# Optimization experiments

Hardware: AMD Instinct MI355X
Metric: run time of the kernel (lower is better)

## Reference

```python
import jax, jax.numpy as jnp
import numpy as np

B, T, NE, H = 4, 1024, 1024, 16
HS = NE // H  # 64
EPS = 0.00064


def setup_inputs() -> dict:
    key = jax.random.key(0)
    ks = jax.random.split(key, 30)
    def rn(k, shape, s):
        return jax.random.normal(k, shape, jnp.float32) * s
    d = {}
    d["x"] = jax.random.normal(ks[0], (B, T, NE), jnp.float32)
    d["time_maa_x"] = jax.random.uniform(ks[1], (NE,), jnp.float32)
    d["time_maa"] = jax.random.uniform(ks[2], (4, 1, 1, NE), jnp.float32)
    d["maa_w1"] = rn(ks[3], (128, NE), 0.02)   # 4 * D_MIX_LORA=32
    d["maa_w2"] = rn(ks[4], (4, 32, NE), 0.02)
    d["decay_w1"] = rn(ks[5], (64, NE), 0.02)
    d["decay_w2"] = rn(ks[6], (64, NE), 0.02)
    d["aaa_w1"] = rn(ks[7], (16, NE), 0.02)
    d["aaa_w2"] = rn(ks[8], (16, NE), 0.02)
    d["kkk_w1"] = rn(ks[9], (16, NE), 0.02)
    d["kkk_w2"] = rn(ks[10], (16, NE), 0.02)
    d["gate_w1"] = rn(ks[11], (128, NE), 0.02)
    d["gate_w2"] = rn(ks[12], (128, NE), 0.02)
    d["ma_w1"] = rn(ks[13], (16, NE), 0.02)
    d["ma_w2"] = rn(ks[14], (16, NE), 0.02)
    d["mk_w1"] = rn(ks[15], (16, NE), 0.02)
    d["mk_w2"] = rn(ks[16], (16, NE), 0.02)
    d["time_decay"] = jnp.linspace(-6.5, -1.5, NE, dtype=jnp.float32)  # decay_speed + 0.5 shape
    d["time_faaaa"] = rn(ks[17], (NE,), 0.02)
    d["time_aaaaa"] = rn(ks[18], (NE,), 0.02)
    d["time_misc_a"] = rn(ks[19], (NE,), 0.02)
    d["time_misc_k"] = rn(ks[20], (NE,), 0.02)
    d["Wr"] = rn(ks[21], (NE, NE), 0.5 / NE ** 0.5)
    d["Wk"] = rn(ks[22], (NE, NE), 0.05 / NE ** 0.5)
    d["Wv"] = rn(ks[23], (NE, NE), 0.5 / NE ** 0.5)
    d["Wo"] = rn(ks[24], (NE, NE), 1.0 / NE ** 0.5)
    d["ln_w"] = jnp.ones((NE,), jnp.float32)
    d["ln_b"] = jnp.zeros((NE,), jnp.float32)
    return d


def _forward(x, time_maa_x, time_maa, maa_w1, maa_w2, decay_w1, decay_w2,
             aaa_w1, aaa_w2, kkk_w1, kkk_w2, gate_w1, gate_w2,
             ma_w1, ma_w2, mk_w1, mk_w2, time_decay, time_faaaa, time_aaaaa,
             time_misc_a, time_misc_k, Wr, Wk, Wv, Wo, ln_w, ln_b):
    Bx, Tx, C = x.shape
    # token-shift delta: xx[t] = x[t-1] - x[t], with x[-1] = 0
    xx = jnp.pad(x, ((0, 0), (1, 0), (0, 0)))[:, :Tx] - x
    mix = x + xx * time_maa_x
    lo = jnp.tanh(jnp.einsum('btc,dc->btd', mix, maa_w1)).reshape(Bx, Tx, 4, 32)
    lo = jnp.einsum('btgk,gkc->gbtc', lo, maa_w2)           # [4,B,T,C]
    xm = x[None] + xx[None] * (lo + time_maa)               # time_maa broadcasts [4,1,1,C]
    xrg, xwa, xk, xv = xm[0], xm[1], xm[2], xm[3]

    r = xrg @ Wr.T
    g = jnp.tanh(xrg @ gate_w1.T) @ gate_w2
    k = xk @ Wk.T
    v = xv @ Wv.T
    w2 = jnp.tanh(xwa @ decay_w1.T) @ decay_w2
    w = -jax.nn.softplus(-(time_decay + w2)) - 0.5
    kk = k + jnp.tanh(xk @ kkk_w1.T) @ kkk_w2
    kkh = kk.reshape(Bx, Tx, H, HS)
    kk = (kkh / jnp.maximum(jnp.linalg.norm(kkh, axis=-1, keepdims=True), 1e-12)).reshape(Bx, Tx, C)
    a = jax.nn.sigmoid(time_aaaaa + (xwa @ aaa_w1.T) @ aaa_w2)
    ma = jax.nn.sigmoid(time_misc_a + (xwa @ ma_w1.T) @ ma_w2)
    k = k * ma + k * a * (1.0 - ma)
    mk = jax.nn.sigmoid(time_misc_k + (xk @ mk_w1.T) @ mk_w2)
    k = k * jnp.exp(w * mk)
    b = -kk * a

    # RWKV7 delta-rule recurrence: per-(B,H) HSxHS matrix state, scan over T
    def to_th(t):
        return t.reshape(Bx, Tx, H, HS).transpose(1, 0, 2, 3)  # [T,B,H,HS]
    qt, wt, kt, vt, at, bt = map(to_th, (r, w, k, v, kk, b))
    wt = jnp.exp(-jnp.exp(wt))

    def step(s, inp):
        q_, w_, k_, v_, a_, b_ = inp
        sa = jnp.einsum('bhij,bhj->bhi', s, a_)
        s = s * w_[:, :, None, :] + sa[..., None] * b_[:, :, None, :] + v_[..., None] * k_[:, :, None, :]
        return s, jnp.einsum('bhij,bhj->bhi', s, q_)

    s0 = jnp.zeros((Bx, H, HS, HS), x.dtype)
    _, y = jax.lax.scan(step, s0, (qt, wt, kt, vt, at, bt))
    y = y.transpose(1, 0, 2, 3).reshape(Bx, Tx, C)

    # GroupNorm with H groups, eps=0.00064
    yg = y.reshape(Bx, Tx, H, HS)
    mu = yg.mean(-1, keepdims=True)
    var = ((yg - mu) ** 2).mean(-1, keepdims=True)
    y = ((yg - mu) / jnp.sqrt(var + EPS)).reshape(Bx, Tx, C) * ln_w + ln_b

    # per-head bonus: (r.k * faaaa) v
    rk = (r.reshape(Bx, Tx, H, HS) * k.reshape(Bx, Tx, H, HS) * time_faaaa.reshape(H, HS)).sum(-1, keepdims=True)
    y = y + (rk * v.reshape(Bx, Tx, H, HS)).reshape(Bx, Tx, C)
    return (y * g) @ Wo.T


def reference(x, time_maa_x, time_maa, maa_w1, maa_w2, decay_w1, decay_w2,
              aaa_w1, aaa_w2, kkk_w1, kkk_w2, gate_w1, gate_w2,
              ma_w1, ma_w2, mk_w1, mk_w2, time_decay, time_faaaa, time_aaaaa,
              time_misc_a, time_misc_k, Wr, Wk, Wv, Wo, ln_w, ln_b):
    return _forward(x, time_maa_x, time_maa, maa_w1, maa_w2, decay_w1, decay_w2,
                    aaa_w1, aaa_w2, kkk_w1, kkk_w2, gate_w1, gate_w2,
                    ma_w1, ma_w2, mk_w1, mk_w2, time_decay, time_faaaa, time_aaaaa,
                    time_misc_a, time_misc_k, Wr, Wk, Wv, Wo, ln_w, ln_b)
```

## Files before the change

### kernel.cpp

```cpp
#include <hip/hip_runtime.h>
#include <cstdint>
#include <cstddef>

#define BB   4
#define TT   1024
#define CC   1024
#define HH   16
#define HSS  64
#define NNtok 4096
#define EPSGN 0.00064f
#define W2TS 192

typedef unsigned short bf16u;
typedef __attribute__((ext_vector_type(8))) short short8;
typedef __attribute__((ext_vector_type(4))) float f32x4;
#define SLOT 4194304ull

__device__ __forceinline__ float bf2f(bf16u u){
  union { unsigned int i; float f; } cv; cv.i = ((unsigned int)u) << 16; return cv.f;
}
__device__ __forceinline__ unsigned short f2bfbits(unsigned int x){
  return (unsigned short)((x + 0x7fffu + ((x >> 16) & 1u)) >> 16);
}
__device__ __forceinline__ bf16u f2bf(float f){
  union { float f; unsigned int i; } cv; cv.f = f;
  return f2bfbits(cv.i);
}
__device__ __forceinline__ void ld4bf(const bf16u* p, float* o){
  ushort4 u = *reinterpret_cast<const ushort4*>(p);
  o[0]=bf2f(u.x); o[1]=bf2f(u.y); o[2]=bf2f(u.z); o[3]=bf2f(u.w);
}
__device__ __forceinline__ void st4bf(bf16u* p, const float* v){
  ushort4 u; u.x=f2bf(v[0]); u.y=f2bf(v[1]); u.z=f2bf(v[2]); u.w=f2bf(v[3]);
  *reinterpret_cast<ushort4*>(p) = u;
}
__device__ __forceinline__ unsigned short f2h(float f){
  union { _Float16 h; unsigned short s; } c; c.h = (_Float16)f; return c.s;
}
__device__ __forceinline__ void st4h(bf16u* p, const float* v){
  ushort4 u; u.x=f2h(v[0]); u.y=f2h(v[1]); u.z=f2h(v[2]); u.w=f2h(v[3]);
  *reinterpret_cast<ushort4*>(p) = u;
}
__device__ __forceinline__ void ld4f(const float* p, float* o){
  float4 v = *reinterpret_cast<const float4*>(p);
  o[0]=v.x; o[1]=v.y; o[2]=v.z; o[3]=v.w;
}
__device__ __forceinline__ float sigm(float x){ return 1.f / (1.f + expf(-x)); }

__device__ __forceinline__ float bflo(unsigned int u){
  union { unsigned int i; float f; } c; c.i = u << 16; return c.f;
}
__device__ __forceinline__ float bfhi(unsigned int u){
  union { unsigned int i; float f; } c; c.i = u & 0xffff0000u; return c.f;
}
__device__ __forceinline__ float hlo(unsigned int u){
  union { unsigned short s; _Float16 h; } c; c.s = (unsigned short)(u & 0xffffu); return (float)c.h;
}
__device__ __forceinline__ float hhi(unsigned int u){
  union { unsigned short s; _Float16 h; } c; c.s = (unsigned short)(u >> 16); return (float)c.h;
}
__device__ __forceinline__ float hval(unsigned short s){
  union { unsigned short s; _Float16 h; } c; c.s = s; return (float)c.h;
}
__device__ __forceinline__ float dot4(const float* x, const float* y){
  return (x[0]*y[0] + x[1]*y[1]) + (x[2]*y[2] + x[3]*y[3]);
}

template<int CTRL>
__device__ __forceinline__ float dpp_add(float v){
  union { float f; int i; } a, b;
  a.f = v;
  b.i = __builtin_amdgcn_update_dpp(0, a.i, CTRL, 0xF, 0xF, true);
  return v + b.f;
}
__device__ __forceinline__ float red16(float v){
  v = dpp_add<0xB1>(v);
  v = dpp_add<0x4E>(v);
  v = dpp_add<0x124>(v);
  v = dpp_add<0x128>(v);
  return v;
}
__device__ __forceinline__ float red32(float v){
  v = red16(v);
  union { float f; int i; } x, y;
  x.f = v; y.f = v;
  asm volatile("" : "+v"(y.i));
  asm volatile("v_permlane16_swap_b32 %0, %1" : "+v"(x.i), "+v"(y.i));
  return x.f + y.f;
}

__global__ __launch_bounds__(256) void k_prep(const float* __restrict__ x,
                                              const float* __restrict__ tmx,
                                              bf16u* __restrict__ MIX){
  int e = (blockIdx.x * 256 + threadIdx.x) * 4;
  int n = e >> 10;
  int c = e & (CC - 1);
  int t = n & (TT - 1);
  float xf[4]; ld4f(x + e, xf);
  float pf[4] = {0.f, 0.f, 0.f, 0.f};
  if (t > 0) ld4f(x + e - CC, pf);
  float tm[4]; ld4f(tmx + c, tm);
  float mv[4];
  #pragma unroll
  for (int i = 0; i < 4; ++i) mv[i] = xf[i] + (pf[i] - xf[i]) * tm[i];
  st4bf(MIX + e, mv);
}

__global__ __launch_bounds__(256) void k_prep_wconv(
    const float* __restrict__ x, const float* __restrict__ tmx,
    bf16u* __restrict__ MIX,
    const float* __restrict__ Wr, const float* __restrict__ Wk,
    const float* __restrict__ Wv,
    const float* __restrict__ maa_w1, const float* __restrict__ gate_w1,
    const float* __restrict__ decay_w1, const float* __restrict__ aaa_w1,
    const float* __restrict__ ma_w1, const float* __restrict__ kkk_w1,
    const float* __restrict__ mk_w1,
    const float* __restrict__ maa_w2, const float* __restrict__ decay_w2,
    bf16u* __restrict__ WrB, bf16u* __restrict__ WkB, bf16u* __restrict__ WvB,
    bf16u* __restrict__ W1B, bf16u* __restrict__ W2TB){
  int tid = threadIdx.x;
  if (blockIdx.x < 4096){
    int e = (blockIdx.x * 256 + tid) * 4;
    int n = e >> 10;
    int c = e & (CC - 1);
    int t = n & (TT - 1);
    float xf[4]; ld4f(x + e, xf);
    float pf[4] = {0.f, 0.f, 0.f, 0.f};
    if (t > 0) ld4f(x + e - CC, pf);
    float tm[4]; ld4f(tmx + c, tm);
    float mv[4];
    #pragma unroll
    for (int i = 0; i < 4; ++i) mv[i] = xf[i] + (pf[i] - xf[i]) * tm[i];
    st4bf(MIX + e, mv);
    return;
  }
  int blk = blockIdx.x - 4096;
  if (blk < 3072){
    const float* src = (blk < 1024) ? Wr : (blk < 2048) ? Wk : Wv;
    bf16u* dst = (blk < 1024) ? WrB : (blk < 2048) ? WkB : WvB;
    size_t e = (size_t)(blk & 1023) * 1024 + (size_t)tid * 4;
    float v[4]; ld4f(src + e, v);
    st4bf(dst + e, v);
  } else if (blk < 3456){
    int row = blk - 3072;
    const float* src;
    if      (row < 128) src = maa_w1   + (size_t)row * 1024;
    else if (row < 256) src = gate_w1  + (size_t)(row - 128) * 1024;
    else if (row < 320) src = decay_w1 + (size_t)(row - 256) * 1024;
    else if (row < 336) src = aaa_w1   + (size_t)(row - 320) * 1024;
    else if (row < 352) src = ma_w1    + (size_t)(row - 336) * 1024;
    else if (row < 368) src = kkk_w1   + (size_t)(row - 352) * 1024;
    else                src = mk_w1    + (size_t)(row - 368) * 1024;
    float v[4]; ld4f(src + tid * 4, v);
    st4bf(W1B + (size_t)row * 1024 + tid * 4, v);
  } else {
    int j = blk - 3456;
    const float* src = (j < 128) ? (maa_w2 + (size_t)j * 1024)
                                 : (decay_w2 + (size_t)(j - 128) * 1024);
    for (int c = tid; c < 1024; c += 256)
      W2TB[(size_t)c * W2TS + j] = f2bf(src[c]);
  }
}

#define B64_AROW 72
#define B64_ASZ (64*72)
#define B64_BSZ (128*72)
template<bool OB>
__device__ __forceinline__ void gemm_b64_body(const bf16u* __restrict__ X,
                                              const bf16u* __restrict__ WB,
                                              void* __restrict__ OUTv,
                                              int Nd, int Kd, int act_n,
                                              short* __restrict__ As,
                                              short* __restrict__ Bs,
                                              int bn0, int bm0){
  const int tid  = threadIdx.x;
  const int lane = tid & 63;
  const int wv   = tid >> 6;
  const int wm   = wv >> 1, wn = wv & 1;
  const int l15  = lane & 15;
  const int quad = lane >> 4;

  f32x4 acc[2][4];
  #pragma unroll
  for (int mi = 0; mi < 2; ++mi)
    #pragma unroll
    for (int ni = 0; ni < 4; ++ni)
      #pragma unroll
      for (int rg = 0; rg < 4; ++rg) acc[mi][ni][rg] = 0.f;

  const int ra = tid >> 2, k0a = (tid & 3) * 16;
  const int rb = tid >> 1, k0b = (tid & 1) * 32;
  const bf16u* xsrc = X + (size_t)(bm0 + ra) * Kd;
  const bf16u* wsrc = (bn0 + rb < Nd) ? WB + (size_t)(bn0 + rb) * Kd : nullptr;

  uint4 xa0 = *(const uint4*)(xsrc + k0a);
  uint4 xa1 = *(const uint4*)(xsrc + k0a + 8);
  uint4 wa0 = make_uint4(0,0,0,0), wa1 = wa0, wa2 = wa0, wa3 = wa0;
  if (wsrc){
    wa0 = *(const uint4*)(wsrc + k0b);
    wa1 = *(const uint4*)(wsrc + k0b + 8);
    wa2 = *(const uint4*)(wsrc + k0b + 16);
    wa3 = *(const uint4*)(wsrc + k0b + 24);
  }
  *(uint4*)&As[ra * B64_AROW + k0a]      = xa0;
  *(uint4*)&As[ra * B64_AROW + k0a + 8]  = xa1;
  *(uint4*)&Bs[rb * B64_AROW + k0b]      = wa0;
  *(uint4*)&Bs[rb * B64_AROW + k0b + 8]  = wa1;
  *(uint4*)&Bs[rb * B64_AROW + k0b + 16] = wa2;
  *(uint4*)&Bs[rb * B64_AROW + k0b + 24] = wa3;
  __syncthreads();

  const int NS = Kd >> 6;
  for (int s = 0; s < NS; ++s){
    const int cur = s & 1;
    if (s + 1 < NS){
      int kb = (s + 1) << 6;
      xa0 = *(const uint4*)(xsrc + kb + k0a);
      xa1 = *(const uint4*)(xsrc + kb + k0a + 8);
      if (wsrc){
        wa0 = *(const uint4*)(wsrc + kb + k0b);
        wa1 = *(const uint4*)(wsrc + kb + k0b + 8);
        wa2 = *(const uint4*)(wsrc + kb + k0b + 16);
        wa3 = *(const uint4*)(wsrc + kb + k0b + 24);
      }
    }
    #pragma unroll
    for (int kk = 0; kk < 64; kk += 32){
      short8 af[2], bfg[4];
      #pragma unroll
      for (int mi = 0; mi < 2; ++mi)
        af[mi] = *(const short8*)&As[cur*B64_ASZ + (wm*32 + mi*16 + l15) * B64_AROW + kk + quad*8];
      #pragma unroll
      for (int ni = 0; ni < 4; ++ni)
        bfg[ni] = *(const short8*)&Bs[cur*B64_BSZ + (wn*64 + ni*16 + l15) * B64_AROW + kk + quad*8];
      #pragma unroll
      for (int mi = 0; mi < 2; ++mi)
        #pragma unroll
        for (int ni = 0; ni < 4; ++ni)
          acc[mi][ni] = __builtin_amdgcn_mfma_f32_16x16x32_bf16(af[mi], bfg[ni], acc[mi][ni], 0, 0, 0);
    }
    if (s + 1 < NS){
      const int nxt = cur ^ 1;
      *(uint4*)&As[nxt*B64_ASZ + ra * B64_AROW + k0a]      = xa0;
      *(uint4*)&As[nxt*B64_ASZ + ra * B64_AROW + k0a + 8]  = xa1;
      *(uint4*)&Bs[nxt*B64_BSZ + rb * B64_AROW + k0b]      = wa0;
      *(uint4*)&Bs[nxt*B64_BSZ + rb * B64_AROW + k0b + 8]  = wa1;
      *(uint4*)&Bs[nxt*B64_BSZ + rb * B64_AROW + k0b + 16] = wa2;
      *(uint4*)&Bs[nxt*B64_BSZ + rb * B64_AROW + k0b + 24] = wa3;
      __syncthreads();
    }
  }

  #pragma unroll
  for (int mi = 0; mi < 2; ++mi){
    #pragma unroll
    for (int ni = 0; ni < 4; ++ni){
      int col = bn0 + wn*64 + ni*16 + l15;
      if (col >= Nd) continue;
      #pragma unroll
      for (int rg = 0; rg < 4; ++rg){
        int row = bm0 + wm*32 + mi*16 + quad*4 + rg;
        float v = acc[mi][ni][rg];
        if (col < act_n) v = tanhf(v);
        if (OB) ((bf16u*)OUTv)[(size_t)row * Nd + col] = f2bf(v);
        else    ((float*)OUTv)[(size_t)row * Nd + col] = v;
      }
    }
  }
}

template<bool OB>
__global__ __launch_bounds__(256) void k_gemm_b64(const bf16u* __restrict__ X,
                                                  const bf16u* __restrict__ WB,
                                                  void* __restrict__ OUTv,
                                                  int Nd, int Kd, int act_n){
  __shared__ short As[2*B64_ASZ];
  __shared__ short Bs[2*B64_BSZ];
  gemm_b64_body<OB>(X, WB, OUTv, Nd, Kd, act_n, As, Bs,
                    blockIdx.x * 128, blockIdx.y * 64);
}

#define B128_SZ (128*40)
template<bool OB>
__device__ __forceinline__ void gemm_b128_body(const bf16u* __restrict__ X,
                                               const bf16u* __restrict__ WB,
                                               void* __restrict__ OUTv,
                                               int Nd, int Kd, int act_n,
                                               short* __restrict__ As,
                                               short* __restrict__ Bs,
                                               int bn0, int bm0){
  const int tid  = threadIdx.x;
  const int lane = tid & 63;
  const int wv   = tid >> 6;
  const int wm   = wv >> 1, wn = wv & 1;
  const int l15  = lane & 15;
  const int quad = lane >> 4;

  f32x4 acc[4][4];
  #pragma unroll
  for (int mi = 0; mi < 4; ++mi)
    #pragma unroll
    for (int ni = 0; ni < 4; ++ni)
      #pragma unroll
      for (int rg = 0; rg < 4; ++rg) acc[mi][ni][rg] = 0.f;

  const int r    = tid >> 1;
  const int half = (tid & 1) * 16;
  const bf16u* wsrc = (bn0 + r < Nd) ? WB + (size_t)(bn0 + r) * Kd : nullptr;
  const bf16u* xsrc = X + (size_t)(bm0 + r) * Kd;

  uint4 xa = *(const uint4*)(xsrc + half);
  uint4 xb = *(const uint4*)(xsrc + half + 8);
  uint4 wa = make_uint4(0,0,0,0), wb = wa;
  if (wsrc){
    wa = *(const uint4*)(wsrc + half);
    wb = *(const uint4*)(wsrc + half + 8);
  }
  *(uint4*)&As[r * 40 + half]     = xa;
  *(uint4*)&As[r * 40 + half + 8] = xb;
  *(uint4*)&Bs[r * 40 + half]     = wa;
  *(uint4*)&Bs[r * 40 + half + 8] = wb;
  __syncthreads();

  const int NK = Kd >> 5;
  for (int k = 0; k < NK; ++k){
    const int cur = k & 1;
    if (k + 1 < NK){
      int k0 = (k + 1) << 5;
      xa = *(const uint4*)(xsrc + k0 + half);
      xb = *(const uint4*)(xsrc + k0 + half + 8);
      if (wsrc){
        wa = *(const uint4*)(wsrc + k0 + half);
        wb = *(const uint4*)(wsrc + k0 + half + 8);
      }
    }
    short8 af[4], bfg[4];
    #pragma unroll
    for (int mi = 0; mi < 4; ++mi)
      af[mi] = *(const short8*)&As[cur*B128_SZ + (wm*64 + mi*16 + l15) * 40 + quad*8];
    #pragma unroll
    for (int ni = 0; ni < 4; ++ni)
      bfg[ni] = *(const short8*)&Bs[cur*B128_SZ + (wn*64 + ni*16 + l15) * 40 + quad*8];
    #pragma unroll
    for (int mi = 0; mi < 4; ++mi)
      #pragma unroll
      for (int ni = 0; ni < 4; ++ni)
        acc[mi][ni] = __builtin_amdgcn_mfma_f32_16x16x32_bf16(af[mi], bfg[ni], acc[mi][ni], 0, 0, 0);
    if (k + 1 < NK){
      const int nxt = cur ^ 1;
      *(uint4*)&As[nxt*B128_SZ + r * 40 + half]     = xa;
      *(uint4*)&As[nxt*B128_SZ + r * 40 + half + 8] = xb;
      *(uint4*)&Bs[nxt*B128_SZ + r * 40 + half]     = wa;
      *(uint4*)&Bs[nxt*B128_SZ + r * 40 + half + 8] = wb;
      __syncthreads();
    }
  }

  #pragma unroll
  for (int mi = 0; mi < 4; ++mi){
    #pragma unroll
    for (int ni = 0; ni < 4; ++ni){
      int col = bn0 + wn*64 + ni*16 + l15;
      if (col >= Nd) continue;
      #pragma unroll
      for (int rg = 0; rg < 4; ++rg){
        int row = bm0 + wm*64 + mi*16 + quad*4 + rg;
        float v = acc[mi][ni][rg];
        if (col < act_n) v = tanhf(v);
        if (OB) ((bf16u*)OUTv)[(size_t)row * Nd + col] = f2bf(v);
        else    ((float*)OUTv)[(size_t)row * Nd + col] = v;
      }
    }
  }
}

__global__ __launch_bounds__(256) void k_gemm_b128_rkv(const bf16u* __restrict__ X0,
                                                       const bf16u* __restrict__ X2,
                                                       const bf16u* __restrict__ X3,
                                                       const bf16u* __restrict__ WrB,
                                                       const bf16u* __restrict__ WkB,
                                                       const bf16u* __restrict__ WvB,
                                                       bf16u* __restrict__ R,
                                                       bf16u* __restrict__ K0,
                                                       bf16u* __restrict__ V){
  __shared__ short As[2*B128_SZ];
  __shared__ short Bs[2*B128_SZ];
  const int z = blockIdx.z;
  const int bn0 = blockIdx.x * 128, bm0 = blockIdx.y * 128;
  if (z == 0)      gemm_b128_body<true>(X0, WrB, R,  CC, CC, 0, As, Bs, bn0, bm0);
  else if (z == 1) gemm_b128_body<true>(X2, WkB, K0, CC, CC, 0, As, Bs, bn0, bm0);
  else             gemm_b128_body<true>(X3, WvB, V,  CC, CC, 0, As, Bs, bn0, bm0);
}

__global__ __launch_bounds__(256) void k_gemm_b64_lora(const bf16u* __restrict__ X0,
                                                       const bf16u* __restrict__ X1,
                                                       const bf16u* __restrict__ X2,
                                                       const bf16u* __restrict__ W1B,
                                                       bf16u* __restrict__ GT,
                                                       bf16u* __restrict__ P1,
                                                       bf16u* __restrict__ P2){
  __shared__ short As[2*B64_ASZ];
  __shared__ short Bs[2*B64_BSZ];
  const int z = blockIdx.z;
  const int bm0 = blockIdx.y * 64;
  if (z == 0)
    gemm_b64_body<true>(X0, W1B + 128*1024, GT, 128, CC, 128, As, Bs, 0, bm0);
  else if (z == 1)
    gemm_b64_body<true>(X1, W1B + 256*1024, P1, 96, CC, 64, As, Bs, 0, bm0);
  else
    gemm_b64_body<true>(X2, W1B + 352*1024, P2, 32, CC, 16, As, Bs, 0, bm0);
}

template<int KD, int EP>
__device__ __forceinline__ void gemm_nn_body(const bf16u* __restrict__ A, int lda,
                                             const bf16u* __restrict__ BT, int koff,
                                             bf16u* __restrict__ OUT,
                                             const float* __restrict__ x,
                                             const float* __restrict__ tma_g,
                                             short* __restrict__ As,
                                             short* __restrict__ Bs,
                                             int bn0, int bm0){
  const int tid  = threadIdx.x;
  const int lane = tid & 63;
  const int wv   = tid >> 6;
  const int wm   = wv >> 1, wn = wv & 1;
  const int l15  = lane & 15;
  const int quad = lane >> 4;

  for (int idx = tid; idx < 128 * (KD / 8); idx += 256){
    int r  = idx / (KD / 8);
    int kc = (idx % (KD / 8)) * 8;
    *(uint4*)&As[r * (KD + 8) + kc] =
        *(const uint4*)(A + (size_t)(bm0 + r) * lda + kc);
  }
  for (int idx = tid; idx < 128 * (KD / 8); idx += 256){
    int cc_ = idx / (KD / 8);
    int kc  = (idx % (KD / 8)) * 8;
    *(uint4*)&Bs[cc_ * (KD + 8) + kc] =
        *(const uint4*)(BT + (size_t)(bn0 + cc_) * W2TS + koff + kc);
  }
  __syncthreads();

  f32x4 acc[4][4];
  #pragma unroll
  for (int mi = 0; mi < 4; ++mi)
    #pragma unroll
    for (int ni = 0; ni < 4; ++ni)
      #pragma unroll
      for (int rg = 0; rg < 4; ++rg) acc[mi][ni][rg] = 0.f;

  #pragma unroll
  for (int kk = 0; kk < KD; kk += 32){
    short8 af[4], bfg[4];
    #pragma unroll
    for (int mi = 0; mi < 4; ++mi)
      af[mi] = *(const short8*)&As[(wm*64 + mi*16 + l15) * (KD + 8) + kk + quad*8];
    #pragma unroll
    for (int ni = 0; ni < 4; ++ni)
      bfg[ni] = *(const short8*)&Bs[(wn*64 + ni*16 + l15) * (KD + 8) + kk + quad*8];
    #pragma unroll
    for (int mi = 0; mi < 4; ++mi)
      #pragma unroll
      for (int ni = 0; ni < 4; ++ni)
        acc[mi][ni] = __builtin_amdgcn_mfma_f32_16x16x32_bf16(af[mi], bfg[ni], acc[mi][ni], 0, 0, 0);
  }

  #pragma unroll
  for (int mi = 0; mi < 4; ++mi){
    #pragma unroll
    for (int ni = 0; ni < 4; ++ni){
      int col = bn0 + wn*64 + ni*16 + l15;
      float tm = (EP == 1) ? tma_g[col] : 0.f;
      #pragma unroll
      for (int rg = 0; rg < 4; ++rg){
        int row = bm0 + wm*64 + mi*16 + quad*4 + rg;
        float v = acc[mi][ni][rg];
        if (EP == 1){
          float xv = x[(size_t)row * CC + col];
          float xp = ((row & (TT - 1)) == 0) ? 0.f : x[(size_t)row * CC + col - CC];
          v = xv + (xp - xv) * (v + tm);
        }
        OUT[(size_t)row * CC + col] = f2bf(v);
      }
    }
  }
}

template<int KD, int EP>
__global__ __launch_bounds__(256) void k_gemm_nn_b(const bf16u* __restrict__ A, int lda,
                                                   const bf16u* __restrict__ BT, int koff,
                                                   bf16u* __restrict__ OUT,
                                                   const float* __restrict__ x,
                                                   const float* __restrict__ tma_g){
  __shared__ short As[128 * (KD + 8)];
  __shared__ short Bs[128 * (KD + 8)];
  gemm_nn_body<KD, EP>(A, lda, BT, koff, OUT, x, tma_g, As, Bs,
                       blockIdx.x * 128, blockIdx.y * 128);
}

__global__ __launch_bounds__(256) void k_gemm_nn_b4(const bf16u* __restrict__ LO,
                                                    const bf16u* __restrict__ BT,
                                                    bf16u* __restrict__ X0base,
                                                    const float* __restrict__ x,
                                                    const float* __restrict__ tmaa){
  __shared__ short As[128 * 40];
  __shared__ short Bs[128 * 40];
  const int z = blockIdx.z;
  gemm_nn_body<32, 1>(LO + z*32, 128, BT, z*32, X0base + (size_t)z*SLOT,
                      x, tmaa + (size_t)z*CC, As, Bs,
                      blockIdx.x * 128, blockIdx.y * 128);
}

template<bool OB>
__global__ __launch_bounds__(256) void k_gemm_mfma(const bf16u* __restrict__ X,
                                                   const float* __restrict__ Wa,
                                                   const float* __restrict__ Wb,
                                                   const float* __restrict__ Wc,
                                                   int na, int nab,
                                                   void* __restrict__ OUTv,
                                                   int Nd, int Kd, int act_n){
  __shared__ short As[128 * 40];
  __shared__ short Bs[128 * 40];
  const int tid  = threadIdx.x;
  const int lane = tid & 63;
  const int wv   = tid >> 6;
  const int wm   = wv >> 1, wn = wv & 1;
  const int bn0  = blockIdx.x * 128;
  const int bm0  = blockIdx.y * 128;
  const int l15  = lane & 15;
  const int quad = lane >> 4;

  f32x4 acc[4][4];
  #pragma unroll
  for (int mi = 0; mi < 4; ++mi)
    #pragma unroll
    for (int ni = 0; ni < 4; ++ni)
      #pragma unroll
      for (int rg = 0; rg < 4; ++rg) acc[mi][ni][rg] = 0.f;

  const int r    = tid >> 1;
  const int half = (tid & 1) * 16;

  int rr = bn0 + r;
  const float* wsrc = nullptr;
  if (rr < na)        wsrc = Wa + (size_t)rr * Kd;
  else if (rr < nab)  wsrc = Wb + (size_t)(rr - na) * Kd;
  else if (rr < Nd)   wsrc = Wc + (size_t)(rr - nab) * Kd;
  const bf16u* xsrc = X + (size_t)(bm0 + r) * Kd;

  for (int k0 = 0; k0 < Kd; k0 += 32){
    uint4 xa = *(const uint4*)(xsrc + k0 + half);
    uint4 xb = *(const uint4*)(xsrc + k0 + half + 8);
    uint4 w0 = make_uint4(0,0,0,0), w1 = w0, w2 = w0, w3 = w0;
    if (wsrc){
      w0 = *(const uint4*)(wsrc + k0 + half);
      w1 = *(const uint4*)(wsrc + k0 + half + 4);
      w2 = *(const uint4*)(wsrc + k0 + half + 8);
      w3 = *(const uint4*)(wsrc + k0 + half + 12);
    }
    union { unsigned short s[8]; uint4 v; } p0, p1;
    p0.s[0]=f2bfbits(w0.x); p0.s[1]=f2bfbits(w0.y); p0.s[2]=f2bfbits(w0.z); p0.s[3]=f2bfbits(w0.w);
    p0.s[4]=f2bfbits(w1.x); p0.s[5]=f2bfbits(w1.y); p0.s[6]=f2bfbits(w1.z); p0.s[7]=f2bfbits(w1.w);
    p1.s[0]=f2bfbits(w2.x); p1.s[1]=f2bfbits(w2.y); p1.s[2]=f2bfbits(w2.z); p1.s[3]=f2bfbits(w2.w);
    p1.s[4]=f2bfbits(w3.x); p1.s[5]=f2bfbits(w3.y); p1.s[6]=f2bfbits(w3.z); p1.s[7]=f2bfbits(w3.w);

    *(uint4*)&As[r * 40 + half]     = xa;
    *(uint4*)&As[r * 40 + half + 8] = xb;
    *(uint4*)&Bs[r * 40 + half]     = p0.v;
    *(uint4*)&Bs[r * 40 + half + 8] = p1.v;
    __syncthreads();

    short8 af[4], bfg[4];
    #pragma unroll
    for (int mi = 0; mi < 4; ++mi)
      af[mi] = *(const short8*)&As[(wm*64 + mi*16 + l15) * 40 + quad*8];
    #pragma unroll
    for (int ni = 0; ni < 4; ++ni)
      bfg[ni] = *(const short8*)&Bs[(wn*64 + ni*16 + l15) * 40 + quad*8];
    #pragma unroll
    for (int mi = 0; mi < 4; ++mi)
      #pragma unroll
      for (int ni = 0; ni < 4; ++ni)
        acc[mi][ni] = __builtin_amdgcn_mfma_f32_16x16x32_bf16(af[mi], bfg[ni], acc[mi][ni], 0, 0, 0);
    __syncthreads();
  }

  #pragma unroll
  for (int mi = 0; mi < 4; ++mi){
    #pragma unroll
    for (int ni = 0; ni < 4; ++ni){
      int col = bn0 + wn*64 + ni*16 + l15;
      if (col >= Nd) continue;
      #pragma unroll
      for (int rg = 0; rg < 4; ++rg){
        int row = bm0 + wm*64 + mi*16 + quad*4 + rg;
        float v = acc[mi][ni][rg];
        if (col < act_n) v = tanhf(v);
        if (OB) ((bf16u*)OUTv)[(size_t)row * Nd + col] = f2bf(v);
        else    ((float*)OUTv)[(size_t)row * Nd + col] = v;
      }
    }
  }
}

template<int KD, int EP>
__global__ __launch_bounds__(256) void k_gemm_nn(const bf16u* __restrict__ A, int lda,
                                                 const float* __restrict__ B,
                                                 bf16u* __restrict__ OUT,
                                                 const float* __restrict__ x,
                                                 const float* __restrict__ tma_g){
  __shared__ short As[128 * (KD + 8)];
  __shared__ short Bs[128 * (KD + 8)];
  const int tid  = threadIdx.x;
  const int lane = tid & 63;
  const int wv   = tid >> 6;
  const int wm   = wv >> 1, wn = wv & 1;
  const int bn0  = blockIdx.x * 128;
  const int bm0  = blockIdx.y * 128;
  const int l15  = lane & 15;
  const int quad = lane >> 4;

  for (int idx = tid; idx < 128 * (KD / 8); idx += 256){
    int r  = idx / (KD / 8);
    int kc = (idx % (KD / 8)) * 8;
    *(uint4*)&As[r * (KD + 8) + kc] =
        *(const uint4*)(A + (size_t)(bm0 + r) * lda + kc);
  }
  for (int idx = tid; idx < KD * 128; idx += 256){
    int k = idx >> 7, c = idx & 127;
    Bs[c * (KD + 8) + k] = (short)f2bf(B[(size_t)k * CC + bn0 + c]);
  }
  __syncthreads();

  f32x4 acc[4][4];
  #pragma unroll
  for (int mi = 0; mi < 4; ++mi)
    #pragma unroll
    for (int ni = 0; ni < 4; ++ni)
      #pragma unroll
      for (int rg = 0; rg < 4; ++rg) acc[mi][ni][rg] = 0.f;

  #pragma unroll
  for (int kk = 0; kk < KD; kk += 32){
    short8 af[4], bfg[4];
    #pragma unroll
    for (int mi = 0; mi < 4; ++mi)
      af[mi] = *(const short8*)&As[(wm*64 + mi*16 + l15) * (KD + 8) + kk + quad*8];
    #pragma unroll
    for (int ni = 0; ni < 4; ++ni)
      bfg[ni] = *(const short8*)&Bs[(wn*64 + ni*16 + l15) * (KD + 8) + kk + quad*8];
    #pragma unroll
    for (int mi = 0; mi < 4; ++mi)
      #pragma unroll
      for (int ni = 0; ni < 4; ++ni)
        acc[mi][ni] = __builtin_amdgcn_mfma_f32_16x16x32_bf16(af[mi], bfg[ni], acc[mi][ni], 0, 0, 0);
  }

  #pragma unroll
  for (int mi = 0; mi < 4; ++mi){
    #pragma unroll
    for (int ni = 0; ni < 4; ++ni){
      int col = bn0 + wn*64 + ni*16 + l15;
      float tm = (EP == 1) ? tma_g[col] : 0.f;
      #pragma unroll
      for (int rg = 0; rg < 4; ++rg){
        int row = bm0 + wm*64 + mi*16 + quad*4 + rg;
        float v = acc[mi][ni][rg];
        if (EP == 1){
          float xv = x[(size_t)row * CC + col];
          float xp = ((row & (TT - 1)) == 0) ? 0.f : x[(size_t)row * CC + col - CC];
          v = xv + (xp - xv) * (v + tm);
        }
        OUT[(size_t)row * CC + col] = f2bf(v);
      }
    }
  }
}

template<int WMODE>
__global__ __launch_bounds__(256) void k_elem(bf16u* __restrict__ K0,
    const bf16u* __restrict__ P1, const bf16u* __restrict__ P2,
    const bf16u* __restrict__ W2A,
    const float* __restrict__ kw2, const float* __restrict__ aw2,
    const float* __restrict__ maw2, const float* __restrict__ mkw2,
    const float* __restrict__ td,  const float* __restrict__ taa,
    const float* __restrict__ tma, const float* __restrict__ tmk,
    const float* __restrict__ faaaa,
    bf16u* __restrict__ KKN, bf16u* __restrict__ Bb, bf16u* __restrict__ UX,
    float* __restrict__ WF,
    bf16u* __restrict__ Rq, float* __restrict__ Dsc, float* __restrict__ RKsc,
    const float* __restrict__ Wo, const float* __restrict__ gate_w2,
    bf16u* __restrict__ WoB, bf16u* __restrict__ GW2T){
  int tid = threadIdx.x;
  if (blockIdx.x >= 1024){
    int blk = blockIdx.x - 1024;
    if (blk < 1024){
      size_t e = ((size_t)blk * 256 + tid) * 4;
      float v[4]; ld4f(Wo + e, v);
      st4bf(WoB + e, v);
    } else {
      int c = (blk - 1024) * 2 + (tid >> 7);
      int j = tid & 127;
      GW2T[(size_t)c * 128 + j] = f2bf(gate_w2[(size_t)j * CC + c]);
    }
    return;
  }
  int n0 = blockIdx.x * 4;
  __shared__ float at_l[4][16], mat_l[4][16], kt_l[4][16], mkt_l[4][16];
  {
    int grp = tid >> 6, q = tid & 63, tt = q >> 4, j = q & 15;
    if (grp == 0)      at_l[tt][j]  = bf2f(P1[(size_t)(n0+tt)*96 + 64 + j]);
    else if (grp == 1) mat_l[tt][j] = bf2f(P1[(size_t)(n0+tt)*96 + 80 + j]);
    else if (grp == 2) kt_l[tt][j]  = bf2f(P2[(size_t)(n0+tt)*32 + j]);
    else               mkt_l[tt][j] = bf2f(P2[(size_t)(n0+tt)*32 + 16 + j]);
  }
  __syncthreads();
  int c  = tid * 4;
  int h  = tid >> 4;
  int lg = tid & 15;

  float kkk[4][4], aa[4][4], mam[4][4], mkm[4][4];
  #pragma unroll
  for (int tt = 0; tt < 4; ++tt)
    #pragma unroll
    for (int i = 0; i < 4; ++i){ kkk[tt][i]=0; aa[tt][i]=0; mam[tt][i]=0; mkm[tt][i]=0; }

  #pragma unroll 4
  for (int j = 0; j < 16; ++j){
    float wk[4], wa[4], wm[4], wq[4];
    ld4f(kw2  + (size_t)j*CC + c, wk);
    ld4f(aw2  + (size_t)j*CC + c, wa);
    ld4f(maw2 + (size_t)j*CC + c, wm);
    ld4f(mkw2 + (size_t)j*CC + c, wq);
    #pragma unroll
    for (int tt = 0; tt < 4; ++tt){
      float s1 = kt_l[tt][j], s2 = at_l[tt][j], s3 = mat_l[tt][j], s4 = mkt_l[tt][j];
      #pragma unroll
      for (int i = 0; i < 4; ++i){
        kkk[tt][i] += s1 * wk[i];
        aa[tt][i]  += s2 * wa[i];
        mam[tt][i] += s3 * wm[i];
        mkm[tt][i] += s4 * wq[i];
      }
    }
  }

  float td4[4], taa4[4], tma4[4], tmk4[4], fa4[4];
  ld4f(td + c, td4); ld4f(taa + c, taa4); ld4f(tma + c, tma4); ld4f(tmk + c, tmk4);
  ld4f(faaaa + c, fa4);

#define ELEM_TOKEN(TT_, E_, A_, B_, KF_, WD_) do{ \
    float k0a[4]; ld4bf(K0 + (E_), k0a); \
    float w2a[4]; ld4bf(W2A + (E_), w2a); \
    float ssq = 0.f; \
    _Pragma("unroll") \
    for (int i = 0; i < 4; ++i){ A_[i] = k0a[i] + kkk[TT_][i]; ssq += A_[i]*A_[i]; } \
    ssq = red16(ssq); \
    float rinv = 1.f / fmaxf(sqrtf(ssq), 1e-12f); \
    float outw_[4]; \
    _Pragma("unroll") \
    for (int i = 0; i < 4; ++i){ \
      float z  = td4[i] + w2a[i]; \
      float nz = -z; \
      float sp = (nz > 15.f) ? nz : log1pf(expf(nz)); \
      float w  = -sp - 0.5f; \
      float av  = sigm(taa4[i] + aa[TT_][i]); \
      float mav = sigm(tma4[i] + mam[TT_][i]); \
      float mkv = sigm(tmk4[i] + mkm[TT_][i]); \
      A_[i] *= rinv; \
      B_[i]  = -A_[i] * av; \
      KF_[i] = k0a[i] * (mav + av * (1.f - mav)) * expf(w * mkv); \
      float ou = -expf(w); \
      outw_[i] = ou; \
      if (WMODE == 1) WD_[i] = __expf(ou);               \
      else            WD_[i] = __expf(hval(f2h(ou)));    \
    } \
    st4bf(Bb + (E_), B_); \
    st4bf(K0 + (E_), KF_); \
    if (WMODE == 1) *(float4*)(WF + (E_)) = make_float4(WD_[0], WD_[1], WD_[2], WD_[3]); \
    else            st4h(UX + (E_), outw_); \
  }while(0)

  #pragma unroll
  for (int p = 0; p < 2; ++p){
    const int ttE = 2*p, ttO = ttE + 1;
    size_t eE = (size_t)(n0 + ttE) * CC + c;
    size_t eO = eE + CC;
    float aE[4], bE[4], kfE[4], wdE[4];
    float aO[4], bO[4], kfO[4], wdO[4];
    ELEM_TOKEN(ttE, eE, aE, bE, kfE, wdE);
    ELEM_TOKEN(ttO, eO, aO, bO, kfO, wdO);
    st4bf(KKN + eE, aE);

    float rE[4], rO[4];
    ld4bf(Rq + eE, rE); ld4bf(Rq + eO, rO);

    float rkE = red16(rE[0]*kfE[0]*fa4[0] + rE[1]*kfE[1]*fa4[1]
                    + rE[2]*kfE[2]*fa4[2] + rE[3]*kfE[3]*fa4[3]);
    float rkO = red16(rO[0]*kfO[0]*fa4[0] + rO[1]*kfO[1]*fa4[1]
                    + rO[2]*kfO[2]*fa4[2] + rO[3]*kfO[3]*fa4[3]);

    float c1 = red16(dot4(bE, aO));
    float d  = red16(dot4(kfE, aO));
    float u1[4];
    #pragma unroll
    for (int i = 0; i < 4; ++i) u1[i] = wdE[i]*aO[i] + c1*aE[i];
    st4bf(KKN + eO, u1);

    float cq = red16(dot4(bE, rE));
    float e1 = red16(dot4(kfE, rE));
    float qe[4];
    #pragma unroll
    for (int i = 0; i < 4; ++i) qe[i] = wdE[i]*rE[i] + cq*aE[i];
    st4bf(Rq + eE, qe);

    float cz  = red16(dot4(bO, rO));
    float e21 = red16(dot4(kfO, rO));
    float z[4];
    #pragma unroll
    for (int i = 0; i < 4; ++i) z[i] = wdO[i]*rO[i] + cz*aO[i];
    float cy  = red16(dot4(bE, z));
    float e20 = red16(dot4(kfE, z));
    float qo[4];
    #pragma unroll
    for (int i = 0; i < 4; ++i) qo[i] = wdE[i]*z[i] + cy*aE[i];
    st4bf(Rq + eO, qo);

    if (lg == 0){
      size_t pr = (size_t)((n0 + ttE) >> 1);
      float4 dv; dv.x = d; dv.y = e1; dv.z = e20; dv.w = e21;
      *(float4*)(Dsc + (pr * HH + h) * 4) = dv;
      RKsc[(size_t)(n0 + ttE) * HH + h] = rkE;
      RKsc[(size_t)(n0 + ttO) * HH + h] = rkO;
    }
  }
#undef ELEM_TOKEN
}

template<int WMODE>
__global__ __launch_bounds__(256) void k_rec(const bf16u* __restrict__ Qp,
                                             const bf16u* __restrict__ WT,
                                             const float* __restrict__ WF,
                                             const bf16u* __restrict__ KFt,
                                             const bf16u* __restrict__ Vt,
                                             const bf16u* __restrict__ Aa,
                                             const bf16u* __restrict__ Bv,
                                             const float* __restrict__ Dsc,
                                             bf16u* __restrict__ Y){
  const int p   = blockIdx.x;
  const int g   = (p & 7) | ((p >> 6) << 3);
  const int oct = (p >> 3) & 7;
  const int b   = g >> 4;
  const int h   = g & 15;
  const int tid = threadIdx.x;
  const int l31 = tid & 31;
  const int i   = oct * 8 + (tid >> 5);
  const size_t base0 = (size_t)(b * TT) * CC + h * HSS;
  const size_t colb  = base0 + l31 * 2;
  const size_t rowb  = base0 + i;
  const size_t dscb  = ((size_t)(b * (TT/2)) * HH + h) * 4;

  float S0 = 0.f, S1 = 0.f;

  unsigned int qEA,qOA,aEA,uOA,kEA,kOA,bEA,bOA,wEA,wOA; float2 fEA,fOA; unsigned short vEA,vOA; float4 dA;
  unsigned int qEB,qOB,aEB,uOB,kEB,kOB,bEB,bOB,wEB,wOB; float2 fEB,fOB; unsigned short vEB,vOB; float4 dB;
  unsigned int qEC,qOC,aEC,uOC,kEC,kOC,bEC,bOC,wEC,wOC; float2 fEC,fOC; unsigned short vEC,vOC; float4 dC;
  unsigned int qED,qOD,aED,uOD,kED,kOD,bED,bOD,wED,wOD; float2 fED,fOD; unsigned short vED,vOD; float4 dD;

#define PL(S, T_) do{ \
    size_t cE_ = colb + (size_t)(T_) * CC, cO_ = cE_ + CC; \
    qE##S = *(const unsigned int*)(Qp  + cE_); qO##S = *(const unsigned int*)(Qp  + cO_); \
    aE##S = *(const unsigned int*)(Aa  + cE_); uO##S = *(const unsigned int*)(Aa  + cO_); \
    kE##S = *(const unsigned int*)(KFt + cE_); kO##S = *(const unsigned int*)(KFt + cO_); \
    bE##S = *(const unsigned int*)(Bv  + cE_); bO##S = *(const unsigned int*)(Bv  + cO_); \
    if (WMODE == 1){ \
      fE##S = *(const float2*)(WF + cE_); fO##S = *(const float2*)(WF + cO_); \
    } else { \
      wE##S = *(const unsigned int*)(WT + cE_); wO##S = *(const unsigned int*)(WT + cO_); \
    } \
    vE##S = Vt[rowb + (size_t)(T_) * CC]; \
    vO##S = Vt[rowb + (size_t)(T_ + 1) * CC]; \
    d##S  = *(const float4*)(Dsc + dscb + (size_t)((T_) >> 1) * (HH*4)); \
  }while(0)

#define PSTEP(S, T_) do{ \
    float a0=bflo(aE##S), a1=bfhi(aE##S); \
    float u0=bflo(uO##S), u1=bfhi(uO##S); \
    float g0=bflo(qE##S), g1=bfhi(qE##S); \
    float o0=bflo(qO##S), o1=bfhi(qO##S); \
    float pE_ = fmaf(S1, a1, S0 * a0); \
    float pO_ = fmaf(S1, u1, S0 * u0); \
    float yE_ = fmaf(S1, g1, S0 * g0); \
    float yO_ = fmaf(S1, o1, S0 * o0); \
    pE_ = red32(pE_); \
    pO_ = red32(pO_); \
    yE_ = red32(yE_); \
    yO_ = red32(yO_); \
    float vEf = bf2f(vE##S), vOf = bf2f(vO##S); \
    float saE = pE_; \
    float saO = fmaf(d##S.x, vEf, pO_); \
    float ypE = fmaf(d##S.y, vEf, yE_); \
    float ypO = fmaf(d##S.z, vEf, fmaf(d##S.w, vOf, yO_)); \
    float k0=bflo(kE##S), k1=bfhi(kE##S); \
    float b0=bflo(bE##S), b1=bfhi(bE##S); \
    float w0, w1; \
    if (WMODE == 1){ w0=fE##S.x; w1=fE##S.y; } \
    else { w0=__expf(hlo(wE##S)); w1=__expf(hhi(wE##S)); } \
    S0 = fmaf(S0, w0, fmaf(saE, b0, vEf * k0)); \
    S1 = fmaf(S1, w1, fmaf(saE, b1, vEf * k1)); \
    float ko0=bflo(kO##S), ko1=bfhi(kO##S); \
    float bo0=bflo(bO##S), bo1=bfhi(bO##S); \
    float wo0, wo1; \
    if (WMODE == 1){ wo0=fO##S.x; wo1=fO##S.y; } \
    else { wo0=__expf(hlo(wO##S)); wo1=__expf(hhi(wO##S)); } \
    S0 = fmaf(S0, wo0, fmaf(saO, bo0, vOf * ko0)); \
    S1 = fmaf(S1, wo1, fmaf(saO, bo1, vOf * ko1)); \
    if (l31 == 0){ \
      Y[rowb + (size_t)(T_) * CC]     = f2bf(ypE); \
      Y[rowb + (size_t)(T_ + 1) * CC] = f2bf(ypO); \
    } \
  }while(0)

  PL(A, 0); PL(B, 2); PL(C, 4); PL(D, 6);
  for (int t = 0; t < TT; t += 8){
    PSTEP(A, t);
    if (t + 8  < TT) PL(A, t + 8);
    PSTEP(B, t + 2);
    if (t + 10 < TT) PL(B, t + 10);
    PSTEP(C, t + 4);
    if (t + 12 < TT) PL(C, t + 12);
    PSTEP(D, t + 6);
    if (t + 14 < TT) PL(D, t + 14);
  }
#undef PL
#undef PSTEP
}

__global__ __launch_bounds__(256) void k_post(const bf16u* __restrict__ Y,
                                              const bf16u* __restrict__ Vt,
                                              const bf16u* __restrict__ GV,
                                              const float* __restrict__ lnw,
                                              const float* __restrict__ lnb,
                                              const float* __restrict__ RKsc,
                                              bf16u* __restrict__ YG){
  int n = blockIdx.x, tid = threadIdx.x;
  int c = tid * 4;
  size_t e = (size_t)n * CC + c;

  float ya[4]; ld4bf(Y + e, ya);
  float s = ya[0] + ya[1] + ya[2] + ya[3];
  s = red16(s);
  float mu = s * (1.f / 64.f);
  float d[4], vs = 0.f;
  #pragma unroll
  for (int i = 0; i < 4; ++i){ d[i] = ya[i] - mu; vs += d[i] * d[i]; }
  vs = red16(vs);
  float rstd = rsqrtf(vs * (1.f / 64.f) + EPSGN);

  float rk = RKsc[(size_t)n * HH + (tid >> 4)];

  float va[4]; ld4bf(Vt + e, va);
  float lw4[4], lb4[4];
  ld4f(lnw + c, lw4); ld4f(lnb + c, lb4);
  float g[4]; ld4bf(GV + e, g);
  float o[4];
  #pragma unroll
  for (int i = 0; i < 4; ++i){
    float yn = d[i] * rstd * lw4[i] + lb4[i] + rk * va[i];
    o[i] = yn * g[i];
  }
  st4bf(YG + e, o);
}

extern "C" void kernel_launch(void* const* d_in, const int* in_sizes, int n_in,
                              void* d_out, int out_size, void* d_ws, size_t ws_size,
                              hipStream_t stream){
  (void)in_sizes; (void)n_in; (void)out_size;
  const float* x        = (const float*)d_in[0];
  const float* tmx      = (const float*)d_in[1];
  const float* tmaa     = (const float*)d_in[2];
  const float* maa_w1   = (const float*)d_in[3];
  const float* maa_w2   = (const float*)d_in[4];
  const float* decay_w1 = (const float*)d_in[5];
  const float* decay_w2 = (const float*)d_in[6];
  const float* aaa_w1   = (const float*)d_in[7];
  const float* aaa_w2   = (const float*)d_in[8];
  const float* kkk_w1   = (const float*)d_in[9];
  const float* kkk_w2   = (const float*)d_in[10];
  const float* gate_w1  = (const float*)d_in[11];
  const float* gate_w2  = (const float*)d_in[12];
  const float* ma_w1    = (const float*)d_in[13];
  const float* ma_w2    = (const float*)d_in[14];
  const float* mk_w1    = (const float*)d_in[15];
  const float* mk_w2    = (const float*)d_in[16];
  const float* t_decay  = (const float*)d_in[17];
  const float* t_faaaa  = (const float*)d_in[18];
  const float* t_aaaaa  = (const float*)d_in[19];
  const float* t_misc_a = (const float*)d_in[20];
  const float* t_misc_k = (const float*)d_in[21];
  const float* Wr       = (const float*)d_in[22];
  const float* Wk       = (const float*)d_in[23];
  const float* Wv       = (const float*)d_in[24];
  const float* Wo       = (const float*)d_in[25];
  const float* ln_w     = (const float*)d_in[26];
  const float* ln_b     = (const float*)d_in[27];

  bf16u* bw  = (bf16u*)d_ws;
  bf16u* MIX = bw + 0*SLOT;
  bf16u* X0  = bw + 0*SLOT;
  bf16u* KKN = bw + 0*SLOT;
  bf16u* YG  = bw + 0*SLOT;
  bf16u* X1  = bw + 1*SLOT;
  bf16u* Bb  = bw + 1*SLOT;
  bf16u* GV  = bw + 1*SLOT;
  bf16u* X2  = bw + 2*SLOT;
  bf16u* UX  = bw + 2*SLOT;
  bf16u* X3  = bw + 3*SLOT;
  bf16u* W2A = bw + 3*SLOT;
  bf16u* Yb  = bw + 3*SLOT;
  bf16u* R   = bw + 4*SLOT;
  bf16u* K0  = bw + 5*SLOT;
  bf16u* V   = bw + 6*SLOT;
  char*  wsb = (char*)d_ws;
  bf16u* LO  = (bf16u*)(wsb + (56ull<<20));
  bf16u* GT  = (bf16u*)(wsb + (57ull<<20));
  bf16u* P1  = (bf16u*)(wsb + (58ull<<20));
  bf16u* P2  = (bf16u*)(wsb + (58ull<<20) + (768ull<<10));
  float* Dsc = (float*)(wsb + (59ull<<20));
  float* RKsc= (float*)(wsb + (59ull<<20) + (512ull<<10));
  float* WF  = (float*)(wsb + (60ull<<20));
  bf16u* WrB = (bf16u*)(wsb + (60ull<<20));
  bf16u* WkB = (bf16u*)(wsb + (62ull<<20));
  bf16u* WvB = (bf16u*)(wsb + (64ull<<20));
  bf16u* W1B = (bf16u*)(wsb + (66ull<<20));
  bf16u* W2TB= (bf16u*)(wsb + (67ull<<20));
  bf16u* WoB = UX;
  bf16u* GW2T= UX + 1048576;
  const bool fast = ws_size >= (77ull<<20);

  if (fast){
    k_prep_wconv<<<7744, 256, 0, stream>>>(x, tmx, MIX,
                                           Wr, Wk, Wv, maa_w1, gate_w1, decay_w1,
                                           aaa_w1, ma_w1, kkk_w1, mk_w1,
                                           maa_w2, decay_w2,
                                           WrB, WkB, WvB, W1B, W2TB);
    k_gemm_b64<true><<<dim3(1,64),256,0,stream>>>(MIX, W1B, LO, 128, CC, 128);
    k_gemm_nn_b4<<<dim3(8,32,4),256,0,stream>>>(LO, W2TB, X0, x, tmaa);
    k_gemm_b128_rkv<<<dim3(8,32,3),256,0,stream>>>(X0, X2, X3, WrB, WkB, WvB,
                                                   R, K0, V);
    k_gemm_b64_lora<<<dim3(1,64,3),256,0,stream>>>(X0, X1, X2, W1B, GT, P1, P2);
    k_gemm_nn_b<64,0><<<dim3(8,32),256,0,stream>>>(P1, 96, W2TB, 128, W2A, nullptr, nullptr);
    k_elem<1><<<2560, 256, 0, stream>>>(K0, P1, P2, W2A,
                                        kkk_w2, aaa_w2, ma_w2, mk_w2,
                                        t_decay, t_aaaaa, t_misc_a, t_misc_k, t_faaaa,
                                        KKN, Bb, UX, WF, R, Dsc, RKsc,
                                        Wo, gate_w2, WoB, GW2T);
    k_rec<1><<<512, 256, 0, stream>>>(R, UX, WF, K0, V, KKN, Bb, Dsc, Yb);
    k_gemm_b64<true><<<dim3(8,64),256,0,stream>>>(GT, GW2T, GV, CC, 128, 0);
    k_post<<<4096, 256, 0, stream>>>(Yb, V, GV, ln_w, ln_b, RKsc, YG);
    k_gemm_b64<false><<<dim3(8,64),256,0,stream>>>(YG, WoB, d_out, CC, CC, 0);
  } else {
    k_prep<<<4096, 256, 0, stream>>>(x, tmx, MIX);
    k_gemm_mfma<true><<<dim3(1,32),256,0,stream>>>(MIX, maa_w1, maa_w1, maa_w1,
                                                   128, 128, LO, 128, CC, 128);
    bf16u* XMs[4] = {X0, X1, X2, X3};
    for (int g = 0; g < 4; ++g)
      k_gemm_nn<32,1><<<dim3(8,32),256,0,stream>>>(LO + g*32, 128,
                                                   maa_w2 + (size_t)g*32*CC,
                                                   XMs[g], x, tmaa + (size_t)g*CC);
    k_gemm_mfma<true><<<dim3(8,32),256,0,stream>>>(X0, Wr, Wr, Wr, CC, CC, R,  CC, CC, 0);
    k_gemm_mfma<true><<<dim3(8,32),256,0,stream>>>(X2, Wk, Wk, Wk, CC, CC, K0, CC, CC, 0);
    k_gemm_mfma<true><<<dim3(8,32),256,0,stream>>>(X3, Wv, Wv, Wv, CC, CC, V,  CC, CC, 0);
    k_gemm_mfma<true><<<dim3(1,32),256,0,stream>>>(X0, gate_w1, gate_w1, gate_w1,
                                                   128, 128, GT, 128, CC, 128);
    k_gemm_mfma<true><<<dim3(1,32),256,0,stream>>>(X1, decay_w1, aaa_w1, ma_w1,
                                                   64, 80, P1, 96, CC, 64);
    k_gemm_mfma<true><<<dim3(1,32),256,0,stream>>>(X2, kkk_w1, mk_w1, mk_w1,
                                                   16, 32, P2, 32, CC, 16);
    k_gemm_nn<64,0><<<dim3(8,32),256,0,stream>>>(P1, 96, decay_w2, W2A, nullptr, nullptr);
    k_elem<0><<<1024, 256, 0, stream>>>(K0, P1, P2, W2A,
                                        kkk_w2, aaa_w2, ma_w2, mk_w2,
                                        t_decay, t_aaaaa, t_misc_a, t_misc_k, t_faaaa,
                                        KKN, Bb, UX, WF, R, Dsc, RKsc,
                                        Wo, gate_w2, WoB, GW2T);
    k_rec<0><<<512, 256, 0, stream>>>(R, UX, WF, K0, V, KKN, Bb, Dsc, Yb);
    k_gemm_nn<128,0><<<dim3(8,32),256,0,stream>>>(GT, 128, gate_w2, GV, nullptr, nullptr);
    k_post<<<4096, 256, 0, stream>>>(Yb, V, GV, ln_w, ln_b, RKsc, YG);
    k_gemm_mfma<false><<<dim3(8,32),256,0,stream>>>(YG, Wo, Wo, Wo, CC, CC, d_out, CC, CC, 0);
  }
}
```

Before: 566.5 us.

## Use direct global-to-LDS loads with XOR swizzle in 128x128 rkv GEMM

Replaces the register-staged global load and LDS store in the 128-tile R/K/V GEMM with global_load_lds instructions that write 16 bytes per lane straight into shared memory. The padded stride-40 layout becomes an unpadded stride-32 layout, with an XOR swizzle on the column chunk applied on both the load and read side to avoid bank conflicts. This is meant to cut register pressure and VALU/LDS store work and to let the prefetch overlap the MFMAs. It relies on the loads finishing before the barrier and on the swizzle mapping matching on both sides. The bounds check on Nd for W rows is also dropped, which is safe here because N is 1024.

```diff
diff --git a/kernel.cpp b/kernel.cpp
--- a/kernel.cpp
+++ b/kernel.cpp
@@ -64,6 +64,13 @@
 }
 __device__ __forceinline__ float dot4(const float* x, const float* y){
   return (x[0]*y[0] + x[1]*y[1]) + (x[2]*y[2] + x[3]*y[3]);
+}
+
+__device__ __forceinline__ void gload_lds16(const bf16u* g, short* l){
+  __builtin_amdgcn_global_load_lds(
+      (const __attribute__((address_space(1))) unsigned int*)g,
+      (__attribute__((address_space(3))) unsigned int*)l,
+      16, 0, 0);
 }
 
 template<int CTRL>
@@ -280,15 +287,15 @@
                     blockIdx.x * 128, blockIdx.y * 64);
 }
 
-#define B128_SZ (128*40)
+#define B128L_SZ (128*32)
 template<bool OB>
-__device__ __forceinline__ void gemm_b128_body(const bf16u* __restrict__ X,
-                                               const bf16u* __restrict__ WB,
-                                               void* __restrict__ OUTv,
-                                               int Nd, int Kd, int act_n,
-                                               short* __restrict__ As,
-                                               short* __restrict__ Bs,
-                                               int bn0, int bm0){
+__device__ __forceinline__ void gemm_b128_lds_body(const bf16u* __restrict__ X,
+                                                   const bf16u* __restrict__ WB,
+                                                   void* __restrict__ OUTv,
+                                                   int Nd, int Kd, int act_n,
+                                                   short* __restrict__ As,
+                                                   short* __restrict__ Bs,
+                                                   int bn0, int bm0){
   const int tid  = threadIdx.x;
   const int lane = tid & 63;
   const int wv   = tid >> 6;
@@ -304,56 +311,49 @@
       #pragma unroll
       for (int rg = 0; rg < 4; ++rg) acc[mi][ni][rg] = 0.f;
 
-  const int r    = tid >> 1;
-  const int half = (tid & 1) * 16;
-  const bf16u* wsrc = (bn0 + r < Nd) ? WB + (size_t)(bn0 + r) * Kd : nullptr;
-  const bf16u* xsrc = X + (size_t)(bm0 + r) * Kd;
-
-  uint4 xa = *(const uint4*)(xsrc + half);
-  uint4 xb = *(const uint4*)(xsrc + half + 8);
-  uint4 wa = make_uint4(0,0,0,0), wb = wa;
-  if (wsrc){
-    wa = *(const uint4*)(wsrc + half);
-    wb = *(const uint4*)(wsrc + half + 8);
-  }
-  *(uint4*)&As[r * 40 + half]     = xa;
-  *(uint4*)&As[r * 40 + half + 8] = xb;
-  *(uint4*)&Bs[r * 40 + half]     = wa;
-  *(uint4*)&Bs[r * 40 + half + 8] = wb;
+  const int srow = lane >> 2;
+  const int cl   = (lane & 3) ^ ((lane >> 3) & 3);
+  const bf16u* gA0 = X  + (size_t)(bm0 + wv*32 + srow)      * Kd + cl*8;
+  const bf16u* gA1 = X  + (size_t)(bm0 + wv*32 + 16 + srow) * Kd + cl*8;
+  const bf16u* gB0 = WB + (size_t)(bn0 + wv*32 + srow)      * Kd + cl*8;
+  const bf16u* gB1 = WB + (size_t)(bn0 + wv*32 + 16 + srow) * Kd + cl*8;
+  short* ldsA0 = As + wv*1024;
+  short* ldsA1 = As + wv*1024 + 512;
+  short* ldsB0 = Bs + wv*1024;
+  short* ldsB1 = Bs + wv*1024 + 512;
+
+  gload_lds16(gA0, ldsA0);
+  gload_lds16(gA1, ldsA1);
+  gload_lds16(gB0, ldsB0);
+  gload_lds16(gB1, ldsB1);
   __syncthreads();
 
+  const int cq = (quad ^ ((l15 >> 1) & 3)) * 8;
   const int NK = Kd >> 5;
   for (int k = 0; k < NK; ++k){
     const int cur = k & 1;
     if (k + 1 < NK){
-      int k0 = (k + 1) << 5;
-      xa = *(const uint4*)(xsrc + k0 + half);
-      xb = *(const uint4*)(xsrc + k0 + half + 8);
-      if (wsrc){
-        wa = *(const uint4*)(wsrc + k0 + half);
-        wb = *(const uint4*)(wsrc + k0 + half + 8);
-      }
+      int ko = (k + 1) << 5;
+      const int nxt = cur ^ 1;
+      gload_lds16(gA0 + ko, ldsA0 + nxt*B128L_SZ);
+      gload_lds16(gA1 + ko, ldsA1 + nxt*B128L_SZ);
+      gload_lds16(gB0 + ko, ldsB0 + nxt*B128L_SZ);
+      gload_lds16(gB1 + ko, ldsB1 + nxt*B128L_SZ);
     }
     short8 af[4], bfg[4];
     #pragma unroll
     for (int mi = 0; mi < 4; ++mi)
-      af[mi] = *(const short8*)&As[cur*B128_SZ + (wm*64 + mi*16 + l15) * 40 + quad*8];
+      af[mi] = *(const short8*)&As[cur*B128L_SZ + (wm*64 + mi*16 + l15) * 32 + cq];
     #pragma unroll
     for (int ni = 0; ni < 4; ++ni)
-      bfg[ni] = *(const short8*)&Bs[cur*B128_SZ + (wn*64 + ni*16 + l15) * 40 + quad*8];
+      bfg[ni] = *(const short8*)&Bs[cur*B128L_SZ + (wn*64 + ni*16 + l15) * 32 + cq];
     #pragma unroll
     for (int mi = 0; mi < 4; ++mi)
       #pragma unroll
       for (int ni = 0; ni < 4; ++ni)
         acc[mi][ni] = __builtin_amdgcn_mfma_f32_16x16x32_bf16(af[mi], bfg[ni], acc[mi][ni], 0, 0, 0);
-    if (k + 1 < NK){
-      const int nxt = cur ^ 1;
-      *(uint4*)&As[nxt*B128_SZ + r * 40 + half]     = xa;
-      *(uint4*)&As[nxt*B128_SZ + r * 40 + half + 8] = xb;
-      *(uint4*)&Bs[nxt*B128_SZ + r * 40 + half]     = wa;
-      *(uint4*)&Bs[nxt*B128_SZ + r * 40 + half + 8] = wb;
+    if (k + 1 < NK)
       __syncthreads();
-    }
   }
 
   #pragma unroll
@@ -383,13 +383,13 @@
                                                        bf16u* __restrict__ R,
                                                        bf16u* __restrict__ K0,
                                                        bf16u* __restrict__ V){
-  __shared__ short As[2*B128_SZ];
-  __shared__ short Bs[2*B128_SZ];
+  __shared__ short As[2*B128L_SZ];
+  __shared__ short Bs[2*B128L_SZ];
   const int z = blockIdx.z;
   const int bn0 = blockIdx.x * 128, bm0 = blockIdx.y * 128;
-  if (z == 0)      gemm_b128_body<true>(X0, WrB, R,  CC, CC, 0, As, Bs, bn0, bm0);
-  else if (z == 1) gemm_b128_body<true>(X2, WkB, K0, CC, CC, 0, As, Bs, bn0, bm0);
-  else             gemm_b128_body<true>(X3, WvB, V,  CC, CC, 0, As, Bs, bn0, bm0);
+  if (z == 0)      gemm_b128_lds_body<true>(X0, WrB, R,  CC, CC, 0, As, Bs, bn0, bm0);
+  else if (z == 1) gemm_b128_lds_body<true>(X2, WkB, K0, CC, CC, 0, As, Bs, bn0, bm0);
+  else             gemm_b128_lds_body<true>(X3, WvB, V,  CC, CC, 0, As, Bs, bn0, bm0);
 }
 
 __global__ __launch_bounds__(256) void k_gemm_b64_lora(const bf16u* __restrict__ X0,
```

Result: no change. 571.9 us (+0.9%).
